# Optimization experiments

Hardware: AMD Instinct MI355X
Metric: run time of the kernel (lower is better)

Reference implementation:

```python
import jax, jax.numpy as jnp
import numpy as np

B, N, C, H, R = 64, 197, 768, 12, 98   # batch, tokens, dim, heads, eliminated tokens
SPARSITY, ALPHA = 0.2, 0.1
EPS = 1e-5  # torch nn.LayerNorm default


def layernorm(x, g, b):
    m = jnp.mean(x, axis=-1, keepdims=True)
    v = jnp.var(x, axis=-1, keepdims=True)
    return (x - m) / jnp.sqrt(v + EPS) * g + b


def setup_inputs() -> dict:
    key = jax.random.key(0)
    ks = jax.random.split(key, 8)
    s = lambda k, sh: (jax.random.normal(k, sh, jnp.float32) * 0.02)
    return dict(
        x=jax.random.normal(ks[0], (B, N, C), jnp.float32),
        norm1_g=jnp.ones((C,), jnp.float32), norm1_b=jnp.zeros((C,), jnp.float32),
        qkv_w=s(ks[1], (C, 3 * C)),                      # qkv_bias=False
        proj_w=s(ks[2], (C, C)), proj_b=jnp.zeros((C,), jnp.float32),
        norm2_g=jnp.ones((C,), jnp.float32), norm2_b=jnp.zeros((C,), jnp.float32),
        fc1_w=s(ks[3], (C, 4 * C)), fc1_b=jnp.zeros((4 * C,), jnp.float32),
        fc2_w=s(ks[4], (4 * C, C)), fc2_b=jnp.zeros((C,), jnp.float32),
    )


def reference(x, norm1_g, norm1_b, qkv_w, proj_w, proj_b,
              norm2_g, norm2_b, fc1_w, fc1_b, fc2_w, fc2_b):
    Dh = C // H
    scale = Dh ** -0.5
    # --- attention block ---
    h = layernorm(x, norm1_g, norm1_b)
    qkv = (h @ qkv_w).reshape(B, N, 3, H, Dh).transpose(2, 0, 3, 1, 4)
    q, k, v = qkv[0] * scale, qkv[1], qkv[2]
    attn = jax.nn.softmax(jnp.einsum('bhnd,bhmd->bhnm', q, k), axis=-1)  # [B,H,N,N]
    out = jnp.einsum('bhnm,bhmd->bhnd', attn, v).transpose(0, 2, 1, 3).reshape(B, N, C)
    x = x + out @ proj_w + proj_b
    # --- selection: DiagAttn (head-mean attention diagonal, excluding CLS) ---
    diag = jnp.diagonal(attn.mean(1), axis1=1, axis2=2)[:, 1:]          # [B, N-1]
    token_rank = jnp.argsort(-diag, axis=1) + 1                          # indices into [1, N)
    nk = N - 1 - R                                                       # kept image tokens
    idx_kept = jnp.sort(jnp.concatenate(
        [jnp.zeros((B, 1), token_rank.dtype), token_rank[:, :nk]], axis=1), axis=1)  # [B, K]
    idx_elim = jnp.sort(token_rank[:, nk:], axis=1)                      # [B, R]
    K = nk + 1
    # --- propagate: ThresholdGraph (multihead=True, threshold=True) ---
    x_kept = jnp.take_along_axis(x, idx_kept[:, :, None], axis=1)        # [B, K, C]
    x_elim = jnp.take_along_axis(x, idx_elim[:, :, None], axis=1)        # [B, R, C]
    w = jnp.take_along_axis(attn, idx_kept[:, None, :, None], axis=2)    # [B,H,K,N]
    w = jnp.take_along_axis(w, idx_elim[:, None, None, :], axis=3)       # [B,H,K,R]
    thr_idx = int(R * K * SPARSITY)
    w_sorted = -jnp.sort(-w.reshape(B, H, K * R), axis=-1)               # descending
    thr = w_sorted[:, :, thr_idx][:, :, None, None]
    w = jnp.where(w >= thr, w, jnp.zeros((), w.dtype))
    x_prop = jnp.einsum('bhke,behd->bkhd', w, x_elim.reshape(B, R, H, Dh)).reshape(B, K, C)
    x = x_kept + ALPHA * x_prop                                          # [B, K, C]
    # --- mlp block ---
    h2 = layernorm(x, norm2_g, norm2_b)
    h2 = jax.nn.gelu(h2 @ fc1_w + fc1_b, approximate=False) @ fc2_w + fc2_b
    return x + h2
```

## Files before the change

kernel.cpp:

```cpp
#include <hip/hip_runtime.h>
#include <math.h>

#define NTOK 197
#define CD   768
#define NH   12
#define DH   64
#define NBATCH 64
#define RTOK 98
#define KTOK 99
#define THRN 1941
#define WTOT (KTOK*RTOK)
#define SROWS 208

typedef __attribute__((ext_vector_type(8))) short short8;
typedef __attribute__((ext_vector_type(8))) unsigned short u16x8;
typedef __attribute__((ext_vector_type(4))) float floatx4;

__device__ __forceinline__ int clamp196(int v){ return ((unsigned)v > 196u) ? 196 : v; }
__device__ __forceinline__ unsigned short f2b(float f){
  unsigned u = __float_as_uint(f);
  return (unsigned short)((u + 0x7FFFu + ((u>>16)&1u)) >> 16);
}
__device__ __forceinline__ float us2f(unsigned short u){ return __uint_as_float(((unsigned)u)<<16); }
__device__ __forceinline__ int swz(int row, int q){ return q ^ (((row>>1)&3)<<3); }

__device__ __forceinline__ void ldsplit(const float* ap, int rem, u16x8& h, u16x8& l){
  float v[8];
  if (rem >= 8) {
    float4 t0 = *(const float4*)ap, t1 = *(const float4*)(ap+4);
    v[0]=t0.x; v[1]=t0.y; v[2]=t0.z; v[3]=t0.w;
    v[4]=t1.x; v[5]=t1.y; v[6]=t1.z; v[7]=t1.w;
  } else {
#pragma unroll
    for (int j=0;j<8;j++) v[j] = (j < rem) ? ap[j] : 0.f;
  }
#pragma unroll
  for (int j=0;j<8;j++){
    unsigned short hh = f2b(v[j]);
    h[j] = hh;
    l[j] = f2b(v[j] - us2f(hh));
  }
}

__global__ __launch_bounds__(256) void fill_kernel(float* __restrict__ out, int n, float val)
{
  int i = blockIdx.x*256 + threadIdx.x;
  if (i < n) out[i] = val;
}

__global__ __launch_bounds__(256) void tcast_k(const float* __restrict__ src, int K, int ldn, int col0,
                                               unsigned short* __restrict__ dst)
{
  __shared__ float t[32][33];
  int n0 = blockIdx.x*32, k0 = blockIdx.y*32;
  int lx = threadIdx.x & 31, ly = threadIdx.x >> 5;
#pragma unroll
  for (int i=0;i<4;i++)
    t[ly + i*8][lx] = src[(long)(k0 + ly + i*8)*ldn + col0 + n0 + lx];
  __syncthreads();
#pragma unroll
  for (int i=0;i<4;i++){
    int n = ly + i*8;
    dst[(long)(n0 + n)*K + k0 + lx] = f2b(t[lx][n]);
  }
}

__global__ __launch_bounds__(256) void tcast3_k(const float* __restrict__ src, int K, int ldn, int col0,
                                                unsigned short* __restrict__ dsth,
                                                unsigned short* __restrict__ dstl)
{
  __shared__ float t[32][33];
  int n0 = blockIdx.x*32, k0 = blockIdx.y*32;
  int lx = threadIdx.x & 31, ly = threadIdx.x >> 5;
#pragma unroll
  for (int i=0;i<4;i++)
    t[ly + i*8][lx] = src[(long)(k0 + ly + i*8)*ldn + col0 + n0 + lx];
  __syncthreads();
#pragma unroll
  for (int i=0;i<4;i++){
    int n = ly + i*8;
    float v = t[lx][n];
    unsigned short h = f2b(v);
    dsth[(long)(n0 + n)*K + k0 + lx] = h;
    dstl[(long)(n0 + n)*K + k0 + lx] = f2b(v - us2f(h));
  }
}

__global__ __launch_bounds__(256) void vtrans_k(const unsigned short* __restrict__ src,
                                                unsigned short* __restrict__ dst)
{
  __shared__ unsigned short t[32][33];
  int z = blockIdx.z;
  int t0 = blockIdx.x*32, d0 = blockIdx.y*32;
  int lx = threadIdx.x & 31, ly = threadIdx.x >> 5;
  const unsigned short* s = src + (long)z*NTOK*DH;
  unsigned short* o = dst + (long)z*DH*NTOK;
#pragma unroll
  for (int i=0;i<4;i++){
    int tok = t0 + ly + i*8;
    t[ly+i*8][lx] = (tok < NTOK) ? s[(long)tok*DH + d0 + lx] : (unsigned short)0;
  }
  __syncthreads();
#pragma unroll
  for (int i=0;i<4;i++){
    int d = d0 + ly + i*8;
    int tok = t0 + lx;
    if (tok < NTOK) o[(long)d*NTOK + tok] = t[lx][ly+i*8];
  }
}

__global__ __launch_bounds__(256) void ln_kernel(const float* __restrict__ xin,
                                                 const float* __restrict__ gam,
                                                 const float* __restrict__ bet,
                                                 unsigned short* __restrict__ outh,
                                                 unsigned short* __restrict__ outl)
{
  int row = blockIdx.x;
  int tid = threadIdx.x;
  long base = (long)row * CD;
  float v[3];
#pragma unroll
  for (int i=0;i<3;i++) v[i] = xin[base + tid + i*256];
  float s  = v[0]+v[1]+v[2];
  float s2 = v[0]*v[0]+v[1]*v[1]+v[2]*v[2];
#pragma unroll
  for (int off=32; off; off>>=1){ s += __shfl_down(s,off); s2 += __shfl_down(s2,off); }
  __shared__ float ps[4], ps2[4], mb[2];
  if ((tid&63)==0){ ps[tid>>6]=s; ps2[tid>>6]=s2; }
  __syncthreads();
  if (tid==0){
    float S  = ps[0]+ps[1]+ps[2]+ps[3];
    float S2 = ps2[0]+ps2[1]+ps2[2]+ps2[3];
    float m  = S / (float)CD;
    float var = S2 / (float)CD - m*m;
    mb[0]=m; mb[1]=1.0f/sqrtf(var + 1e-5f);
  }
  __syncthreads();
  float m=mb[0], inv=mb[1];
#pragma unroll
  for (int i=0;i<3;i++){
    int c = tid + i*256;
    float r = (v[i]-m)*inv*gam[c] + bet[c];
    unsigned short h = f2b(r);
    outh[base+c] = h;
    if (outl) outl[base+c] = f2b(r - us2f(h));
  }
}

__global__ __launch_bounds__(256) void sqs_k(const unsigned short* __restrict__ Qh,
                                             const unsigned short* __restrict__ Ql,
                                             const unsigned short* __restrict__ Kh,
                                             const unsigned short* __restrict__ Kl,
                                             float* __restrict__ S)
{
  __shared__ short Bh_s[SROWS*64], Bl_s[SROWS*64];
  int tid = threadIdx.x;
  int z = blockIdx.y;
  int m0 = blockIdx.x * 128;
  const unsigned short* qhz = Qh + (long)z*NTOK*DH;
  const unsigned short* qlz = Ql + (long)z*NTOK*DH;
  const unsigned short* khz = Kh + (long)z*NTOK*DH;
  const unsigned short* klz = Kl + (long)z*NTOK*DH;
  u16x8 zz = {0,0,0,0,0,0,0,0};
  for (int i = tid; i < SROWS*8; i += 256) {
    int row = i>>3, c = i&7;
    u16x8 vh = zz, vl = zz;
    if (row < NTOK) {
      vh = *(const u16x8*)(khz + (long)row*DH + c*8);
      vl = *(const u16x8*)(klz + (long)row*DH + c*8);
    }
    int off = row*64 + ((c ^ (row&7))<<3);
    *(u16x8*)&Bh_s[off] = vh;
    *(u16x8*)&Bl_s[off] = vl;
  }
  __syncthreads();
  int w = tid>>6, l = tid&63;
  int lr = l&15, hi2 = l>>4, kq = hi2*8;
  int rbase0 = m0 + (w<<5);
  floatx4 acc[2][13];
#pragma unroll
  for (int mt=0;mt<2;mt++)
#pragma unroll
    for (int nt=0;nt<13;nt++) acc[mt][nt] = (floatx4){0.f,0.f,0.f,0.f};
#pragma unroll
  for (int ks=0; ks<2; ks++){
    int k0 = ks*32;
    short8 afh[2], afl[2];
#pragma unroll
    for (int mt=0;mt<2;mt++){
      int rowA = clamp196(rbase0 + mt*16 + lr);
      long qo = (long)rowA*DH + k0 + kq;
      afh[mt] = *(const short8*)(qhz + qo);
      afl[mt] = *(const short8*)(qlz + qo);
    }
#pragma unroll
    for (int nt=0;nt<13;nt++){
      int rowB = nt*16 + lr;
      int cc = (ks<<2) + hi2;
      int off = rowB*64 + ((cc ^ (rowB&7))<<3);
      short8 bfh = *(short8*)&Bh_s[off];
      short8 bfl = *(short8*)&Bl_s[off];
#pragma unroll
      for (int mt=0;mt<2;mt++){
        acc[mt][nt] = __builtin_amdgcn_mfma_f32_16x16x32_bf16(afh[mt], bfh, acc[mt][nt], 0, 0, 0);
        acc[mt][nt] = __builtin_amdgcn_mfma_f32_16x16x32_bf16(afh[mt], bfl, acc[mt][nt], 0, 0, 0);
        acc[mt][nt] = __builtin_amdgcn_mfma_f32_16x16x32_bf16(afl[mt], bfh, acc[mt][nt], 0, 0, 0);
      }
    }
  }
  float* Sz = S + (long)z*NTOK*NTOK;
#pragma unroll
  for (int mt=0;mt<2;mt++){
#pragma unroll
    for (int r=0;r<4;r++){
      int row = rbase0 + mt*16 + hi2*4 + r;
      float ev[13];
      float mx = -3.4e38f;
#pragma unroll
      for (int nt=0;nt<13;nt++){
        int col = nt*16 + lr;
        float v = acc[mt][nt][r];
        if (col >= NTOK) v = -3.4e38f;
        ev[nt] = v;
        mx = fmaxf(mx, v);
      }
#pragma unroll
      for (int mk=1; mk<16; mk<<=1) mx = fmaxf(mx, __shfl_xor(mx, mk));
      float sum = 0.f;
#pragma unroll
      for (int nt=0;nt<13;nt++){
        float e = expf(ev[nt]-mx);
        ev[nt] = e;
        sum += e;
      }
#pragma unroll
      for (int mk=1; mk<16; mk<<=1) sum += __shfl_xor(sum, mk);
      if (row < NTOK){
#pragma unroll
        for (int nt=0;nt<13;nt++){
          int col = nt*16 + lr;
          if (col < NTOK) Sz[(long)row*NTOK + col] = ev[nt]/sum;
        }
      }
    }
  }
}

struct PvP {
  const float* P;
  const unsigned short* Vt;
  unsigned short* C;
};

__global__ __launch_bounds__(256) void pv_k(PvP p)
{
  __shared__ short Ahs[128*32], Als[128*32], Bs[64*32];
  int tid = threadIdx.x;
  int z = blockIdx.z;
  int cb = z / NH, h = z - cb*NH;
  const float* Az = p.P + (long)z*NTOK*NTOK;
  const unsigned short* Bz = p.Vt + (long)z*DH*NTOK;
  int m0 = blockIdx.y*128;
  int w = tid>>6, l = tid&63;
  int wm = (w&1)*64, wn = (w>>1)*32;
  int lr = l&15, kq = (l>>4)*8;
  floatx4 acc[4][2];
#pragma unroll
  for (int i=0;i<4;i++)
#pragma unroll
    for (int j=0;j<2;j++) acc[i][j] = (floatx4){0.f,0.f,0.f,0.f};
  int r0i = tid>>2, q0 = (tid&3)*8;
  int r1i = r0i + 64;
  int w0s = swz(r0i, q0), w1s = swz(r1i, q0);
  for (int k0 = 0; k0 < NTOK; k0 += 32) {
    u16x8 ah0={0,0,0,0,0,0,0,0}, al0={0,0,0,0,0,0,0,0};
    u16x8 ah1={0,0,0,0,0,0,0,0}, al1={0,0,0,0,0,0,0,0};
    u16x8 b0 ={0,0,0,0,0,0,0,0};
    int rem = NTOK - k0 - q0;
    { int gm = m0 + r0i;
      if (gm < NTOK && rem > 0) ldsplit(Az + (long)gm*NTOK + k0 + q0, rem, ah0, al0); }
    { int gm = m0 + r1i;
      if (gm < NTOK && rem > 0) ldsplit(Az + (long)gm*NTOK + k0 + q0, rem, ah1, al1); }
    { const unsigned short* bp = Bz + (long)r0i*NTOK + k0 + q0;
      if (rem >= 8) b0 = *(const u16x8*)bp;
      else if (rem > 0) {
#pragma unroll
        for (int j=0;j<8;j++) if (j < rem) b0[j] = bp[j];
      } }
    __syncthreads();
    *(u16x8*)&Ahs[r0i*32 + w0s] = ah0;
    *(u16x8*)&Ahs[r1i*32 + w1s] = ah1;
    *(u16x8*)&Als[r0i*32 + w0s] = al0;
    *(u16x8*)&Als[r1i*32 + w1s] = al1;
    *(u16x8*)&Bs [r0i*32 + w0s] = b0;
    __syncthreads();
    short8 afh[4], afl[4], bfr[2];
#pragma unroll
    for (int mt=0;mt<4;mt++){
      int rr = wm + mt*16 + lr; int rs = rr*32 + swz(rr,kq);
      afh[mt] = *(short8*)&Ahs[rs];
      afl[mt] = *(short8*)&Als[rs];
    }
#pragma unroll
    for (int nt=0;nt<2;nt++){
      int rr = wn + nt*16 + lr;
      bfr[nt] = *(short8*)&Bs[rr*32 + swz(rr,kq)];
    }
#pragma unroll
    for (int mt=0;mt<4;mt++)
#pragma unroll
      for (int nt=0;nt<2;nt++){
        acc[mt][nt] = __builtin_amdgcn_mfma_f32_16x16x32_bf16(afh[mt], bfr[nt], acc[mt][nt], 0, 0, 0);
        acc[mt][nt] = __builtin_amdgcn_mfma_f32_16x16x32_bf16(afl[mt], bfr[nt], acc[mt][nt], 0, 0, 0);
      }
  }
  int rbase = (l>>4)*4;
#pragma unroll
  for (int mt=0;mt<4;mt++){
#pragma unroll
    for (int r=0;r<4;r++){
      int gm = m0 + wm + mt*16 + rbase + r;
      if (gm >= NTOK) continue;
#pragma unroll
      for (int nt=0;nt<2;nt++){
        int gn = wn + nt*16 + lr;
        p.C[(long)cb*NTOK*CD + (long)gm*CD + h*DH + gn] = f2b(acc[mt][nt][r]);
      }
    }
  }
}

struct MmP {
  const unsigned short* A;
  const unsigned short* B;
  void* C;
  const float* bias;
  const float* resid;
  unsigned short* vout;
  int M, N, K, ldc;
};

template<int EPI>
__global__ __launch_bounds__(256) void mgemm_k(MmP p)
{
  __shared__ short As[128*32];
  __shared__ short Bs[128*32];
  int tid = threadIdx.x;
  int m0 = blockIdx.y*128, n0 = blockIdx.x*128;
  int w = tid>>6, l = tid&63;
  int wm = (w&1)*64, wn = (w>>1)*64;
  int lr = l&15, kq = (l>>4)*8;
  floatx4 acc[4][4];
#pragma unroll
  for (int i=0;i<4;i++)
#pragma unroll
    for (int j=0;j<4;j++) acc[i][j] = (floatx4){0.f,0.f,0.f,0.f};
  int r0i = tid>>2, q0 = (tid&3)*8;
  int r1i = r0i + 64;
  int w0s = swz(r0i, q0), w1s = swz(r1i, q0);
  for (int k0 = 0; k0 < p.K; k0 += 32) {
    u16x8 a0 = {0,0,0,0,0,0,0,0}, a1 = {0,0,0,0,0,0,0,0};
    { int gm = m0 + r0i;
      if (gm < p.M) a0 = *(const u16x8*)(p.A + (long)gm*p.K + k0 + q0); }
    { int gm = m0 + r1i;
      if (gm < p.M) a1 = *(const u16x8*)(p.A + (long)gm*p.K + k0 + q0); }
    u16x8 b0 = *(const u16x8*)(p.B + (long)(n0 + r0i)*p.K + k0 + q0);
    u16x8 b1 = *(const u16x8*)(p.B + (long)(n0 + r1i)*p.K + k0 + q0);
    __syncthreads();
    *(u16x8*)&As[r0i*32 + w0s] = a0;
    *(u16x8*)&As[r1i*32 + w1s] = a1;
    *(u16x8*)&Bs[r0i*32 + w0s] = b0;
    *(u16x8*)&Bs[r1i*32 + w1s] = b1;
    __syncthreads();
    short8 af[4], bfr[4];
#pragma unroll
    for (int mt=0;mt<4;mt++){ int rr = wm + mt*16 + lr; af[mt]  = *(short8*)&As[rr*32 + swz(rr,kq)]; }
#pragma unroll
    for (int nt=0;nt<4;nt++){ int rr = wn + nt*16 + lr; bfr[nt] = *(short8*)&Bs[rr*32 + swz(rr,kq)]; }
#pragma unroll
    for (int mt=0;mt<4;mt++)
#pragma unroll
      for (int nt=0;nt<4;nt++)
        acc[mt][nt] = __builtin_amdgcn_mfma_f32_16x16x32_bf16(af[mt], bfr[nt], acc[mt][nt], 0, 0, 0);
  }
  int rbase = (l>>4)*4;
#pragma unroll
  for (int mt=0;mt<4;mt++){
#pragma unroll
    for (int r=0;r<4;r++){
      int gm = m0 + wm + mt*16 + rbase + r;
      if (gm >= p.M) continue;
#pragma unroll
      for (int nt=0;nt<4;nt++){
        int gn = n0 + wn + nt*16 + lr;
        float val = acc[mt][nt][r];
        if (EPI == 1) {
          int cb = gm / NTOK, tok = gm - cb*NTOK;
          int h = gn >> 6, d = gn & 63;
          p.vout[(((long)cb*NH + h)*NTOK + tok)*DH + d] = f2b(val);
        } else if (EPI == 2) {
          ((float*)p.C)[(long)gm*p.ldc + gn] = val + p.bias[gn] + p.resid[(long)gm*p.ldc + gn];
        } else {
          float u = val + p.bias[gn];
          ((unsigned short*)p.C)[(long)gm*p.ldc + gn] = f2b(0.5f*u*(1.0f + erff(u*0.70710678118654752f)));
        }
      }
    }
  }
}

struct Mm3P {
  const unsigned short *Ah, *Al, *Bh, *Bl;
  float* C;
  unsigned short *qh, *ql, *kh, *kl;
  long az, bz, cz;
  int M, N, K, ldc;
};

template<int EPI>
__global__ __launch_bounds__(256) void mgemm3_k(Mm3P p)
{
  __shared__ short Ahs[128*32], Als[128*32], Bhs[128*32], Bls[128*32];
  int tid = threadIdx.x;
  int z = blockIdx.z;
  const unsigned short* Azh = p.Ah + (long)z*p.az;
  const unsigned short* Azl = p.Al + (long)z*p.az;
  const unsigned short* Bzh = p.Bh + (long)z*p.bz;
  const unsigned short* Bzl = p.Bl + (long)z*p.bz;
  int m0 = blockIdx.y*128, n0 = blockIdx.x*128;
  int w = tid>>6, l = tid&63;
  int wm = (w&1)*64, wn = (w>>1)*64;
  int lr = l&15, kq = (l>>4)*8;
  floatx4 acc[4][4];
#pragma unroll
  for (int i=0;i<4;i++)
#pragma unroll
    for (int j=0;j<4;j++) acc[i][j] = (floatx4){0.f,0.f,0.f,0.f};
  int r0i = tid>>2, q0 = (tid&3)*8;
  int r1i = r0i + 64;
  int w0s = swz(r0i, q0), w1s = swz(r1i, q0);
  for (int k0 = 0; k0 < p.K; k0 += 32) {
    u16x8 ah0={0,0,0,0,0,0,0,0}, al0={0,0,0,0,0,0,0,0};
    u16x8 ah1={0,0,0,0,0,0,0,0}, al1={0,0,0,0,0,0,0,0};
    u16x8 bh0={0,0,0,0,0,0,0,0}, bl0={0,0,0,0,0,0,0,0};
    u16x8 bh1={0,0,0,0,0,0,0,0}, bl1={0,0,0,0,0,0,0,0};
    { int gm = m0 + r0i;
      if (gm < p.M) {
        long o = (long)gm*p.K + k0 + q0;
        ah0 = *(const u16x8*)(Azh + o);
        al0 = *(const u16x8*)(Azl + o);
      } }
    { int gm = m0 + r1i;
      if (gm < p.M) {
        long o = (long)gm*p.K + k0 + q0;
        ah1 = *(const u16x8*)(Azh + o);
        al1 = *(const u16x8*)(Azl + o);
      } }
    { int gn = n0 + r0i;
      if (gn < p.N) {
        long o = (long)gn*p.K + k0 + q0;
        bh0 = *(const u16x8*)(Bzh + o);
        bl0 = *(const u16x8*)(Bzl + o);
      } }
    { int gn = n0 + r1i;
      if (gn < p.N) {
        long o = (long)gn*p.K + k0 + q0;
        bh1 = *(const u16x8*)(Bzh + o);
        bl1 = *(const u16x8*)(Bzl + o);
      } }
    __syncthreads();
    *(u16x8*)&Ahs[r0i*32 + w0s] = ah0;
    *(u16x8*)&Ahs[r1i*32 + w1s] = ah1;
    *(u16x8*)&Als[r0i*32 + w0s] = al0;
    *(u16x8*)&Als[r1i*32 + w1s] = al1;
    *(u16x8*)&Bhs[r0i*32 + w0s] = bh0;
    *(u16x8*)&Bhs[r1i*32 + w1s] = bh1;
    *(u16x8*)&Bls[r0i*32 + w0s] = bl0;
    *(u16x8*)&Bls[r1i*32 + w1s] = bl1;
    __syncthreads();
    short8 afh[4], afl[4], bfh[4], bfl[4];
#pragma unroll
    for (int mt=0;mt<4;mt++){
      int rr = wm + mt*16 + lr; int rs = rr*32 + swz(rr,kq);
      afh[mt] = *(short8*)&Ahs[rs];
      afl[mt] = *(short8*)&Als[rs];
    }
#pragma unroll
    for (int nt=0;nt<4;nt++){
      int rr = wn + nt*16 + lr; int rs = rr*32 + swz(rr,kq);
      bfh[nt] = *(short8*)&Bhs[rs];
      bfl[nt] = *(short8*)&Bls[rs];
    }
#pragma unroll
    for (int mt=0;mt<4;mt++)
#pragma unroll
      for (int nt=0;nt<4;nt++){
        acc[mt][nt] = __builtin_amdgcn_mfma_f32_16x16x32_bf16(afh[mt], bfh[nt], acc[mt][nt], 0, 0, 0);
        acc[mt][nt] = __builtin_amdgcn_mfma_f32_16x16x32_bf16(afh[mt], bfl[nt], acc[mt][nt], 0, 0, 0);
        acc[mt][nt] = __builtin_amdgcn_mfma_f32_16x16x32_bf16(afl[mt], bfh[nt], acc[mt][nt], 0, 0, 0);
      }
  }
  int rbase = (l>>4)*4;
#pragma unroll
  for (int mt=0;mt<4;mt++){
#pragma unroll
    for (int r=0;r<4;r++){
      int gm = m0 + wm + mt*16 + rbase + r;
      if (gm >= p.M) continue;
#pragma unroll
      for (int nt=0;nt<4;nt++){
        int gn = n0 + wn + nt*16 + lr;
        if (gn >= p.N) continue;
        float val = acc[mt][nt][r];
        if (EPI == 0) {
          p.C[(long)z*p.cz + (long)gm*p.ldc + gn] = val;
        } else {
          int which = (gn >= CD) ? 1 : 0;
          int rc = gn - which*CD;
          int hd = rc >> 6, dd = rc & 63;
          int cb = gm / NTOK, tok = gm - cb*NTOK;
          long off = (((long)cb*NH + hd)*NTOK + tok)*DH + dd;
          float v = which ? val : val*0.125f;
          unsigned short h = f2b(v);
          unsigned short lo16 = f2b(v - us2f(h));
          if (which) { p.kh[off] = h; p.kl[off] = lo16; }
          else       { p.qh[off] = h; p.ql[off] = lo16; }
        }
      }
    }
  }
}

__global__ __launch_bounds__(256) void select_kernel(const float* __restrict__ attn,
                                                     int* __restrict__ idx_kept,
                                                     int* __restrict__ idx_elim, int b0)
{
  int cb = blockIdx.x, tid = threadIdx.x;
  int b = b0 + cb;
  __shared__ float diag[NTOK-1];
  __shared__ int kept[NTOK];
  if (tid < NTOK-1) {
    int t = tid + 1;
    float s = 0.f;
#pragma unroll
    for (int h=0; h<NH; h++)
      s += attn[(((long)cb*NH + h)*NTOK + t)*NTOK + t];
    diag[tid] = s / 12.0f;
  }
  if (tid < KTOK) idx_kept[b*KTOK + tid] = 0;
  if (tid < RTOK) idx_elim[b*RTOK + tid] = 1;
  __syncthreads();
  if (tid < NTOK-1) {
    float dv = diag[tid];
    int r = 0;
    for (int m=0; m<NTOK-1; m++){
      float dm = diag[m];
      r += ((dm > dv) || (dm == dv && m < tid)) ? 1 : 0;
    }
    kept[tid+1] = (r < (NTOK-1-RTOK)) ? 1 : 0;
  }
  __syncthreads();
  if (tid < NTOK-1) {
    int t = tid + 1;
    if (kept[t]) {
      int pos = 1;
      for (int s2=1; s2<t; s2++) pos += kept[s2];
      if (pos >= 1 && pos < KTOK) idx_kept[b*KTOK + pos] = t;
    } else {
      int pos = 0;
      for (int s2=1; s2<t; s2++) pos += 1 - kept[s2];
      if (pos >= 0 && pos < RTOK) idx_elim[b*RTOK + pos] = t;
    }
  }
  if (tid == 0) idx_kept[b*KTOK] = 0;
}

#define PNEL 38
__global__ __launch_bounds__(256) void prop_kernel(const float* __restrict__ attn,
                                                   const float* __restrict__ x1c,
                                                   const int* __restrict__ idx_kept,
                                                   const int* __restrict__ idx_elim,
                                                   float* __restrict__ x2, int b0)
{
  int z = blockIdx.x;
  int cb = z / NH, h = z - cb*NH;
  int b = b0 + cb;
  int tid = threadIdx.x;
  int wid = tid >> 6, l = tid & 63;
  int lr = l & 15, hi2 = l >> 4;
  __shared__ short WhL[112*128];
  __shared__ short XtL[64*128];
  __shared__ unsigned hist[64];
  __shared__ int kidx[KTOK], eidx[RTOK];
  if (tid < KTOK) kidx[tid] = clamp196(idx_kept[b*KTOK + tid]);
  if (tid < RTOK) eidx[tid] = clamp196(idx_elim[b*RTOK + tid]);
  u16x8 zz = {0,0,0,0,0,0,0,0};
#pragma unroll
  for (int i=0;i<7;i++) *(u16x8*)&WhL[tid*8 + i*2048] = zz;
#pragma unroll
  for (int i=0;i<4;i++) *(u16x8*)&XtL[tid*8 + i*2048] = zz;
  __syncthreads();
  for (int i = tid; i < RTOK*DH; i += 256){
    int e = i >> 6, d = i & 63;
    float v = x1c[((long)cb*NTOK + eidx[e])*CD + h*DH + d];
    XtL[d*128 + (((e>>3) ^ (d&7))<<3) + (e&7)] = (short)f2b(v);
  }
  const float* ab = attn + (long)z*NTOK*NTOK;
  unsigned wb[PNEL];
#pragma unroll
  for (int j=0;j<PNEL;j++){
    int i = tid + (j<<8);
    if (i < WTOT){
      int k = i / RTOK, e = i - k*RTOK;
      wb[j] = __float_as_uint(ab[kidx[k]*NTOK + eidx[e]]);
    } else wb[j] = 0u;
  }
  unsigned P = 0; int rrank = THRN;
  for (int pass=0; pass<5; ++pass){
    int sh = 24 - 6*pass;
    if (tid < 64) hist[tid] = 0u;
    __syncthreads();
#pragma unroll
    for (int j=0;j<PNEL;j++){
      int i = tid + (j<<8);
      unsigned v = wb[j];
      bool m = (i < WTOT) && ((pass == 0) || ((v >> (sh+6)) == P));
      if (m) atomicAdd(&hist[(v>>sh)&63u], 1u);
    }
    __syncthreads();
    unsigned cum = 0; int bsel = 0; unsigned above = 0;
    for (int bb=63; bb>=0; --bb){
      unsigned hv = hist[bb];
      if (cum + hv >= (unsigned)rrank){ bsel = bb; above = cum; break; }
      cum += hv;
    }
    P = (P<<6) | (unsigned)bsel;
    rrank -= (int)above;
    __syncthreads();
  }
  unsigned thrbits = P;
#pragma unroll
  for (int j=0;j<PNEL;j++){
    int i = tid + (j<<8);
    if (i < WTOT){
      int k = i / RTOK, e = i - k*RTOK;
      unsigned v = (wb[j] >= thrbits) ? wb[j] : 0u;
      WhL[k*128 + (((e>>3) ^ (k&7))<<3) + (e&7)] = (short)f2b(__uint_as_float(v));
    }
  }
  __syncthreads();
  floatx4 acc[7];
#pragma unroll
  for (int mt=0;mt<7;mt++) acc[mt] = (floatx4){0.f,0.f,0.f,0.f};
  short8 bfr[4];
#pragma unroll
  for (int ks=0;ks<4;ks++){
    int c = ks*4 + hi2;
    int rd = wid*16 + lr;
    bfr[ks] = *(short8*)&XtL[rd*128 + ((c ^ (lr&7))<<3)];
  }
#pragma unroll
  for (int mt=0;mt<7;mt++){
#pragma unroll
    for (int ks=0;ks<4;ks++){
      int c = ks*4 + hi2;
      int rw = mt*16 + lr;
      short8 af = *(short8*)&WhL[rw*128 + ((c ^ (lr&7))<<3)];
      acc[mt] = __builtin_amdgcn_mfma_f32_16x16x32_bf16(af, bfr[ks], acc[mt], 0, 0, 0);
    }
  }
#pragma unroll
  for (int mt=0;mt<7;mt++){
#pragma unroll
    for (int r=0;r<4;r++){
      int kt = mt*16 + hi2*4 + r;
      if (kt >= KTOK) continue;
      int d = wid*16 + lr;
      float xk = x1c[((long)cb*NTOK + kidx[kt])*CD + h*DH + d];
      x2[((long)b*KTOK + kt)*CD + h*DH + d] = xk + 0.1f*acc[mt][r];
    }
  }
}

extern "C" void kernel_launch(void* const* d_in, const int* in_sizes, int n_in,
                              void* d_out, int out_size, void* d_ws, size_t ws_size,
                              hipStream_t stream)
{
  const float* x     = (const float*)d_in[0];
  const float* n1g   = (const float*)d_in[1];
  const float* n1b   = (const float*)d_in[2];
  const float* qkvw  = (const float*)d_in[3];
  const float* projw = (const float*)d_in[4];
  const float* projb = (const float*)d_in[5];
  const float* n2g   = (const float*)d_in[6];
  const float* n2b   = (const float*)d_in[7];
  const float* fc1w  = (const float*)d_in[8];
  const float* fc1b  = (const float*)d_in[9];
  const float* fc2w  = (const float*)d_in[10];
  const float* fc2b  = (const float*)d_in[11];
  float* out = (float*)d_out;

  const long XROW = (long)NTOK*CD;
  const long AH   = (long)NTOK*NTOK;
  const long AB   = (long)NH*AH;
  const long SMALL = 6336L + 6272L;
  const long WFIX  = 1769472L;
  const long PB = AB + 3*XROW + XROW/2;
  const long MLPFIX = 2359296L;
  const long MINREQ = SMALL + WFIX + (MLPFIX + 64*1920L > PB ? MLPFIX + 64*1920L : PB);

  long wsf = (long)(ws_size / 4);
  if (wsf < MINREQ) {
    float val = (float)(ws_size >> 20) * 1000.0f + 1.0f;
    fill_kernel<<<dim3((out_size+255)/256), 256, 0, stream>>>(out, out_size, val);
    return;
  }

  long avail = wsf - SMALL - WFIX;
  int G = (int)(avail / PB);
  if (G > NBATCH) G = NBATCH;
  if (G < 1) G = 1;
  long rcl = ((avail - MLPFIX) / 1920L) / 64L * 64L;
  int RC = (int)(rcl > 6336L ? 6336L : rcl);
  if (RC < 64) RC = 64;

  float* ws = (float*)d_ws;
  int*   idx_kept = (int*)ws;
  int*   idx_elim = idx_kept + 6336;
  unsigned short* qkwh   = (unsigned short*)(ws + SMALL);
  unsigned short* qkwl   = qkwh + 1179648;
  unsigned short* qkvwvT = qkwl + 1179648;
  unsigned short* projwT = qkvwvT + 589824;
  float* base  = ws + SMALL + WFIX;
  float* attnc = base;
  unsigned short* qh = (unsigned short*)(base + (long)G*AB);
  unsigned short* ql = qh + (long)G*XROW;
  float* x1c = (float*)qh;
  unsigned short* kh = (unsigned short*)(base + (long)G*AB + (long)G*XROW);
  unsigned short* kl = kh + (long)G*XROW;
  unsigned short* aoutb = kh;
  unsigned short* vc = (unsigned short*)(base + (long)G*AB + 2L*G*XROW);
  unsigned short* h1h = (unsigned short*)(base + (long)G*AB + 2L*G*XROW + (long)G*XROW/2);
  unsigned short* h1l = h1h + (long)G*XROW;
  unsigned short* vt  = h1h;
  unsigned short* fc1wT = (unsigned short*)base;
  unsigned short* fc2wT = fc1wT + 2359296;
  unsigned short* h2b   = (unsigned short*)(base + MLPFIX);
  unsigned short* gb    = h2b + (long)RC*CD;

  tcast3_k<<<dim3(48,24), 256, 0, stream>>>(qkvw, CD, 3*CD, 0, qkwh, qkwl);
  tcast_k <<<dim3(24,24), 256, 0, stream>>>(qkvw, CD, 3*CD, 2*CD, qkvwvT);
  tcast_k <<<dim3(24,24), 256, 0, stream>>>(projw, CD, CD, 0, projwT);

  for (int b0 = 0; b0 < NBATCH; b0 += G) {
    int GL = (NBATCH - b0 < G) ? (NBATCH - b0) : G;
    int MROW = GL*NTOK;
    ln_kernel<<<dim3(MROW), 256, 0, stream>>>(x + (long)b0*XROW, n1g, n1b, h1h, h1l);
    {
      Mm3P p{}; p.Ah=h1h; p.Al=h1l; p.Bh=qkwh; p.Bl=qkwl;
      p.qh=qh; p.ql=ql; p.kh=kh; p.kl=kl;
      p.M=MROW; p.N=2*CD; p.K=CD; p.ldc=0; p.az=0; p.bz=0; p.cz=0;
      mgemm3_k<1><<<dim3(12,(MROW+127)/128,1), 256, 0, stream>>>(p);
    }
    {
      MmP p{}; p.A=h1h; p.B=qkvwvT; p.vout=vc;
      p.M=MROW; p.N=CD; p.K=CD; p.ldc=CD;
      mgemm_k<1><<<dim3(6,(MROW+127)/128,1), 256, 0, stream>>>(p);
    }
    vtrans_k<<<dim3(7,2,GL*NH), 256, 0, stream>>>(vc, vt);
    sqs_k<<<dim3(2, GL*NH), 256, 0, stream>>>(qh, ql, kh, kl, attnc);
    select_kernel<<<dim3(GL), 256, 0, stream>>>(attnc, idx_kept, idx_elim, b0);
    {
      PvP p{}; p.P=attnc; p.Vt=vt; p.C=aoutb;
      pv_k<<<dim3(1,2,GL*NH), 256, 0, stream>>>(p);
    }
    {
      MmP p{}; p.A=aoutb; p.B=projwT; p.C=x1c;
      p.M=MROW; p.N=CD; p.K=CD; p.ldc=CD;
      p.bias=projb; p.resid=x + (long)b0*XROW;
      mgemm_k<2><<<dim3(6,(MROW+127)/128,1), 256, 0, stream>>>(p);
    }
    prop_kernel<<<dim3(GL*NH), 256, 0, stream>>>(attnc, x1c, idx_kept, idx_elim, out, b0);
  }

  tcast_k<<<dim3(96,24), 256, 0, stream>>>(fc1w, CD, 4*CD, 0, fc1wT);
  tcast_k<<<dim3(24,96), 256, 0, stream>>>(fc2w, 4*CD, CD, 0, fc2wT);

  for (int r0 = 0; r0 < NBATCH*KTOK; r0 += RC) {
    int RCL = (NBATCH*KTOK - r0 < RC) ? (NBATCH*KTOK - r0) : RC;
    ln_kernel<<<dim3(RCL), 256, 0, stream>>>(out + (long)r0*CD, n2g, n2b, h2b, nullptr);
    {
      MmP p{}; p.A=h2b; p.B=fc1wT; p.C=gb;
      p.M=RCL; p.N=4*CD; p.K=CD; p.ldc=4*CD; p.bias=fc1b;
      mgemm_k<3><<<dim3(24,(RCL+127)/128,1), 256, 0, stream>>>(p);
    }
    {
      MmP p{}; p.A=gb; p.B=fc2wT; p.C=out + (long)r0*CD;
      p.M=RCL; p.N=CD; p.K=4*CD; p.ldc=CD;
      p.bias=fc2b; p.resid=out + (long)r0*CD;
      mgemm_k<2><<<dim3(6,(RCL+127)/128,1), 256, 0, stream>>>(p);
    }
  }
}
```

Baseline: 712.2 us.

## Emit split-bf16 attention probabilities from softmax and widen GEMM K-tile to 64

The softmax kernel now also writes the attention probabilities as hi/lo bf16 pairs, so the PV kernel loads bf16 directly instead of reading fp32 and splitting in registers. The generic GEMM's K-step grows from 32 to 64 with a new swizzled LDS layout, halving the barrier count per output tile. In exchange the workspace per batch group needs an extra attention-sized buffer, which may shrink the group size G or force more batch iterations, and the softmax kernel writes more bytes overall.

```diff
diff --git a/kernel.cpp b/kernel.cpp
--- a/kernel.cpp
+++ b/kernel.cpp
@@ -151,7 +151,9 @@
                                              const unsigned short* __restrict__ Ql,
                                              const unsigned short* __restrict__ Kh,
                                              const unsigned short* __restrict__ Kl,
-                                             float* __restrict__ S)
+                                             float* __restrict__ S,
+                                             unsigned short* __restrict__ Ph,
+                                             unsigned short* __restrict__ Pl)
 {
   __shared__ short Bh_s[SROWS*64], Bl_s[SROWS*64];
   int tid = threadIdx.x;
@@ -208,7 +210,10 @@
       }
     }
   }
-  float* Sz = S + (long)z*NTOK*NTOK;
+  const long AHL = (long)NTOK*NTOK;
+  float* Sz = S + (long)z*AHL;
+  unsigned short* phz = Ph + (long)z*AHL;
+  unsigned short* plz = Pl + (long)z*AHL;
 #pragma unroll
   for (int mt=0;mt<2;mt++){
 #pragma unroll
@@ -239,7 +244,14 @@
 #pragma unroll
         for (int nt=0;nt<13;nt++){
           int col = nt*16 + lr;
-          if (col < NTOK) Sz[(long)row*NTOK + col] = ev[nt]/sum;
+          if (col < NTOK){
+            float val = ev[nt]/sum;
+            long o = (long)row*NTOK + col;
+            Sz[o] = val;
+            unsigned short hh = f2b(val);
+            phz[o] = hh;
+            plz[o] = f2b(val - us2f(hh));
+          }
         }
       }
     }
@@ -247,7 +259,8 @@
 }
 
 struct PvP {
-  const float* P;
+  const unsigned short* Ph;
+  const unsigned short* Pl;
   const unsigned short* Vt;
   unsigned short* C;
 };
@@ -258,7 +271,9 @@
   int tid = threadIdx.x;
   int z = blockIdx.z;
   int cb = z / NH, h = z - cb*NH;
-  const float* Az = p.P + (long)z*NTOK*NTOK;
+  const long AHL = (long)NTOK*NTOK;
+  const unsigned short* Phz = p.Ph + (long)z*AHL;
+  const unsigned short* Plz = p.Pl + (long)z*AHL;
   const unsigned short* Bz = p.Vt + (long)z*DH*NTOK;
   int m0 = blockIdx.y*128;
   int w = tid>>6, l = tid&63;
@@ -278,9 +293,25 @@
     u16x8 b0 ={0,0,0,0,0,0,0,0};
     int rem = NTOK - k0 - q0;
     { int gm = m0 + r0i;
-      if (gm < NTOK && rem > 0) ldsplit(Az + (long)gm*NTOK + k0 + q0, rem, ah0, al0); }
+      if (gm < NTOK && rem > 0){
+        const unsigned short* hp = Phz + (long)gm*NTOK + k0 + q0;
+        const unsigned short* lp = Plz + (long)gm*NTOK + k0 + q0;
+        if (rem >= 8){ ah0 = *(const u16x8*)hp; al0 = *(const u16x8*)lp; }
+        else {
+#pragma unroll
+          for (int j=0;j<8;j++) if (j < rem){ ah0[j]=hp[j]; al0[j]=lp[j]; }
+        }
+      } }
     { int gm = m0 + r1i;
-      if (gm < NTOK && rem > 0) ldsplit(Az + (long)gm*NTOK + k0 + q0, rem, ah1, al1); }
+      if (gm < NTOK && rem > 0){
+        const unsigned short* hp = Phz + (long)gm*NTOK + k0 + q0;
+        const unsigned short* lp = Plz + (long)gm*NTOK + k0 + q0;
+        if (rem >= 8){ ah1 = *(const u16x8*)hp; al1 = *(const u16x8*)lp; }
+        else {
+#pragma unroll
+          for (int j=0;j<8;j++) if (j < rem){ ah1[j]=hp[j]; al1[j]=lp[j]; }
+        }
+      } }
     { const unsigned short* bp = Bz + (long)r0i*NTOK + k0 + q0;
       if (rem >= 8) b0 = *(const u16x8*)bp;
       else if (rem > 0) {
@@ -343,47 +374,56 @@
 template<int EPI>
 __global__ __launch_bounds__(256) void mgemm_k(MmP p)
 {
-  __shared__ short As[128*32];
-  __shared__ short Bs[128*32];
+  __shared__ short As[128*64];
+  __shared__ short Bs[128*64];
   int tid = threadIdx.x;
   int m0 = blockIdx.y*128, n0 = blockIdx.x*128;
   int w = tid>>6, l = tid&63;
   int wm = (w&1)*64, wn = (w>>1)*64;
-  int lr = l&15, kq = (l>>4)*8;
+  int lr = l&15, hi2 = l>>4;
   floatx4 acc[4][4];
 #pragma unroll
   for (int i=0;i<4;i++)
 #pragma unroll
     for (int j=0;j<4;j++) acc[i][j] = (floatx4){0.f,0.f,0.f,0.f};
-  int r0i = tid>>2, q0 = (tid&3)*8;
-  int r1i = r0i + 64;
-  int w0s = swz(r0i, q0), w1s = swz(r1i, q0);
-  for (int k0 = 0; k0 < p.K; k0 += 32) {
-    u16x8 a0 = {0,0,0,0,0,0,0,0}, a1 = {0,0,0,0,0,0,0,0};
-    { int gm = m0 + r0i;
-      if (gm < p.M) a0 = *(const u16x8*)(p.A + (long)gm*p.K + k0 + q0); }
-    { int gm = m0 + r1i;
-      if (gm < p.M) a1 = *(const u16x8*)(p.A + (long)gm*p.K + k0 + q0); }
-    u16x8 b0 = *(const u16x8*)(p.B + (long)(n0 + r0i)*p.K + k0 + q0);
-    u16x8 b1 = *(const u16x8*)(p.B + (long)(n0 + r1i)*p.K + k0 + q0);
+  int ra = tid>>1, cb4 = (tid&1)*4;
+  int sw = ra & 7;
+  bool mok = (m0 + ra) < p.M;
+  long aoff = (long)(mok ? (m0+ra) : 0)*p.K + cb4*8;
+  long boff = (long)(n0+ra)*p.K + cb4*8;
+  for (int k0 = 0; k0 < p.K; k0 += 64) {
+    u16x8 av[4], bv[4];
+#pragma unroll
+    for (int j=0;j<4;j++){ av[j] = (u16x8){0,0,0,0,0,0,0,0}; }
+    if (mok) {
+#pragma unroll
+      for (int j=0;j<4;j++) av[j] = *(const u16x8*)(p.A + aoff + k0 + j*8);
+    }
+#pragma unroll
+    for (int j=0;j<4;j++) bv[j] = *(const u16x8*)(p.B + boff + k0 + j*8);
     __syncthreads();
-    *(u16x8*)&As[r0i*32 + w0s] = a0;
-    *(u16x8*)&As[r1i*32 + w1s] = a1;
-    *(u16x8*)&Bs[r0i*32 + w0s] = b0;
-    *(u16x8*)&Bs[r1i*32 + w1s] = b1;
+#pragma unroll
+    for (int j=0;j<4;j++){
+      int c = (cb4 + j) ^ sw;
+      *(u16x8*)&As[ra*64 + (c<<3)] = av[j];
+      *(u16x8*)&Bs[ra*64 + (c<<3)] = bv[j];
+    }
     __syncthreads();
-    short8 af[4], bfr[4];
-#pragma unroll
-    for (int mt=0;mt<4;mt++){ int rr = wm + mt*16 + lr; af[mt]  = *(short8*)&As[rr*32 + swz(rr,kq)]; }
-#pragma unroll
-    for (int nt=0;nt<4;nt++){ int rr = wn + nt*16 + lr; bfr[nt] = *(short8*)&Bs[rr*32 + swz(rr,kq)]; }
-#pragma unroll
-    for (int mt=0;mt<4;mt++)
-#pragma unroll
-      for (int nt=0;nt<4;nt++)
-        acc[mt][nt] = __builtin_amdgcn_mfma_f32_16x16x32_bf16(af[mt], bfr[nt], acc[mt][nt], 0, 0, 0);
-  }
-  int rbase = (l>>4)*4;
+#pragma unroll
+    for (int g=0; g<2; g++){
+      short8 af[4], bfr[4];
+#pragma unroll
+      for (int mt=0;mt<4;mt++){ int rr = wm + mt*16 + lr; int c = (g*4+hi2) ^ (rr&7); af[mt] = *(short8*)&As[rr*64 + (c<<3)]; }
+#pragma unroll
+      for (int nt=0;nt<4;nt++){ int rr = wn + nt*16 + lr; int c = (g*4+hi2) ^ (rr&7); bfr[nt] = *(short8*)&Bs[rr*64 + (c<<3)]; }
+#pragma unroll
+      for (int mt=0;mt<4;mt++)
+#pragma unroll
+        for (int nt=0;nt<4;nt++)
+          acc[mt][nt] = __builtin_amdgcn_mfma_f32_16x16x32_bf16(af[mt], bfr[nt], acc[mt][nt], 0, 0, 0);
+    }
+  }
+  int rbase = hi2*4;
 #pragma unroll
   for (int mt=0;mt<4;mt++){
 #pragma unroll
@@ -705,7 +745,7 @@
   const long AB   = (long)NH*AH;
   const long SMALL = 6336L + 6272L;
   const long WFIX  = 1769472L;
-  const long PB = AB + 3*XROW + XROW/2;
+  const long PB = 2*AB + 3*XROW + XROW/2;
   const long MLPFIX = 2359296L;
   const long MINREQ = SMALL + WFIX + (MLPFIX + 64*1920L > PB ? MLPFIX + 64*1920L : PB);
 
@@ -743,6 +783,8 @@
   unsigned short* h1h = (unsigned short*)(base + (long)G*AB + 2L*G*XROW + (long)G*XROW/2);
   unsigned short* h1l = h1h + (long)G*XROW;
   unsigned short* vt  = h1h;
+  unsigned short* ph = (unsigned short*)(base + (long)G*AB + 3L*G*XROW + (long)G*XROW/2);
+  unsigned short* pl = ph + (long)G*AB;
   unsigned short* fc1wT = (unsigned short*)base;
   unsigned short* fc2wT = fc1wT + 2359296;
   unsigned short* h2b   = (unsigned short*)(base + MLPFIX);
@@ -768,10 +810,10 @@
       mgemm_k<1><<<dim3(6,(MROW+127)/128,1), 256, 0, stream>>>(p);
     }
     vtrans_k<<<dim3(7,2,GL*NH), 256, 0, stream>>>(vc, vt);
-    sqs_k<<<dim3(2, GL*NH), 256, 0, stream>>>(qh, ql, kh, kl, attnc);
+    sqs_k<<<dim3(2, GL*NH), 256, 0, stream>>>(qh, ql, kh, kl, attnc, ph, pl);
     select_kernel<<<dim3(GL), 256, 0, stream>>>(attnc, idx_kept, idx_elim, b0);
     {
-      PvP p{}; p.P=attnc; p.Vt=vt; p.C=aoutb;
+      PvP p{}; p.Ph=ph; p.Pl=pl; p.Vt=vt; p.C=aoutb;
       pv_k<<<dim3(1,2,GL*NH), 256, 0, stream>>>(p);
     }
     {
```

After: 880.2 us. 1.24x slower.
